# Optimization experiments

Measured on AMD Instinct MI355X. Metric: run time of the kernel, lower is better.

## Reference

```python
import jax, jax.numpy as jnp
import numpy as np

L = 3          # num_layer
EMB = 128      # emb_dim
NODE_F = 32    # node_feat_dim
EDGE_F = 16    # edge_feat_dim
TASKS = 1
N_GRAPHS = 64
EPS = 1e-5     # BatchNorm eps


def setup_inputs() -> dict:
    key = jax.random.key(0)
    ks = jax.random.split(key, 16)
    N, E = 50000, 800000
    x = jax.random.normal(ks[0], (N, NODE_F), dtype=jnp.float32)
    edge_index = jax.random.randint(ks[1], (2, E), 0, N, dtype=jnp.int32)
    edge_attr = jax.random.normal(ks[2], (E, EDGE_F), dtype=jnp.float32)
    batch = jnp.sort(jax.random.randint(ks[3], (N,), 0, N_GRAPHS, dtype=jnp.int32))
    s = lambda *sh: 1.0 / np.sqrt(sh[-1])
    # input node embedding
    W0 = jax.random.normal(ks[4], (EMB, NODE_F), dtype=jnp.float32) * s(EMB, NODE_F)
    b0 = jnp.zeros((EMB,), jnp.float32)
    # per-layer params, stacked over L
    We = jax.random.normal(ks[5], (L, EMB, EDGE_F), dtype=jnp.float32) * s(EMB, EDGE_F)
    be = jnp.zeros((L, EMB), jnp.float32)
    W1 = jax.random.normal(ks[6], (L, 2 * EMB, EMB), dtype=jnp.float32) * s(2 * EMB, EMB)
    b1 = jnp.zeros((L, 2 * EMB), jnp.float32)
    W2 = jax.random.normal(ks[7], (L, EMB, 2 * EMB), dtype=jnp.float32) * s(EMB, 2 * EMB)
    b2 = jnp.zeros((L, EMB), jnp.float32)
    gamma = jnp.ones((L, EMB), jnp.float32)
    beta = jnp.zeros((L, EMB), jnp.float32)
    # graph prediction head
    Wp = jax.random.normal(ks[8], (TASKS, EMB), dtype=jnp.float32) * s(TASKS, EMB)
    bp = jnp.zeros((TASKS,), jnp.float32)
    return {"x": x, "edge_attr": edge_attr, "W0": W0, "b0": b0, "We": We, "be": be,
            "W1": W1, "b1": b1, "W2": W2, "b2": b2, "gamma": gamma, "beta": beta,
            "Wp": Wp, "bp": bp, "edge_index": edge_index, "batch": batch}


def _forward(x, edge_attr, W0, b0, We, be, W1, b1, W2, b2, gamma, beta, Wp, bp,
             edge_index, batch):
    N = x.shape[0]
    src, dst = edge_index[0], edge_index[1]
    self_idx = jnp.arange(N, dtype=src.dtype)
    src_full = jnp.concatenate([src, self_idx])  # [E+N] with self loops
    dst_full = jnp.concatenate([dst, self_idx])
    h = x @ W0.T + b0  # [N, EMB]
    for l in range(L):
        # edge embedding; self-loop edge_attr is zeros -> embedding is just bias
        e_emb = edge_attr @ We[l].T + be[l]                       # [E, EMB]
        e_self = jnp.broadcast_to(be[l], (N, EMB))                # [N, EMB]
        msgs = h[src_full] + jnp.concatenate([e_emb, e_self], 0)  # [E+N, EMB]
        aggr = jax.ops.segment_sum(msgs, dst_full, num_segments=N)
        h2 = jax.nn.relu(aggr @ W1[l].T + b1[l]) @ W2[l].T + b2[l]
        # BatchNorm1d (training-mode batch statistics, biased var)
        mu = jnp.mean(h2, axis=0)
        var = jnp.mean(jnp.square(h2 - mu), axis=0)
        h = gamma[l] * (h2 - mu) * jax.lax.rsqrt(var + EPS) + beta[l]
        if l < L - 1:
            h = jax.nn.relu(h)
    # global mean pool over graphs
    sums = jax.ops.segment_sum(h, batch, num_segments=N_GRAPHS)
    cnts = jax.ops.segment_sum(jnp.ones((N,), h.dtype), batch, num_segments=N_GRAPHS)
    pooled = sums / jnp.maximum(cnts, 1.0)[:, None]
    return pooled @ Wp.T + bp  # [N_GRAPHS, TASKS]


def reference(x, edge_attr, W0, b0, We, be, W1, b1, W2, b2, gamma, beta, Wp, bp,
              edge_index, batch):
    return _forward(x, edge_attr, W0, b0, We, be, W1, b1, W2, b2, gamma, beta,
                    Wp, bp, edge_index, batch)
```

## Files before the change

### kernel.cpp

```cpp
#include <hip/hip_runtime.h>
#include <stdint.h>

#define EMB 128
#define LAYERS 3
#define NGRAPHS 64
#define BN_EPS 1e-5f

#define BSH 6
#define BNODES 64
#define SUBCAP 256
#define BCAP (8 * SUBCAP + 256)
#define OVFCAP 8192

typedef short short8 __attribute__((ext_vector_type(8)));
typedef float float4v __attribute__((ext_vector_type(4)));
typedef unsigned short ushort4v __attribute__((ext_vector_type(4)));

__device__ __forceinline__ unsigned short f2bf(float f) {
    union { float f; unsigned int i; } v; v.f = f;
    unsigned int x = v.i;
    unsigned int r = x + 0x7FFFu + ((x >> 16) & 1u);
    return (unsigned short)(r >> 16);
}
__device__ __forceinline__ float bflo(unsigned int u) {
    union { unsigned int i; float f; } v; v.i = u << 16; return v.f;
}
__device__ __forceinline__ float bfhi(unsigned int u) {
    union { unsigned int i; float f; } v; v.i = u & 0xffff0000u; return v.f;
}
__device__ __forceinline__ unsigned int packbf(float a, float b) {
    return (unsigned int)f2bf(a) | ((unsigned int)f2bf(b) << 16);
}

__global__ __launch_bounds__(256) void conv_bf16_3(
    const float* __restrict__ a, unsigned short* __restrict__ oa, int na,
    const float* __restrict__ b, unsigned short* __restrict__ ob, int nb,
    const float* __restrict__ c, unsigned short* __restrict__ oc, int nc)
{
    int i = blockIdx.x * 256 + threadIdx.x;
    int stride = gridDim.x * 256;
    for (int t = i; t < na + nb + nc; t += stride) {
        if (t < na) oa[t] = f2bf(a[t]);
        else if (t < na + nb) ob[t - na] = f2bf(b[t - na]);
        else oc[t - na - nb] = f2bf(c[t - na - nb]);
    }
}

template<int K, bool A_IS_BF16, bool RELU, bool OUT_BF16>
__global__ __launch_bounds__(256) void gemm_bt(
    const void* __restrict__ Av, const unsigned short* __restrict__ B,
    const float* __restrict__ bias, void* __restrict__ Cv,
    int M, int Ntot)
{
    const int wave = threadIdx.x >> 6;
    const int lane = threadIdx.x & 63;
    const int q    = lane >> 4;
    const int ln   = lane & 15;
    const int m_base = blockIdx.x * 64 + wave * 16;
    const int n_base = blockIdx.y * 64;

    float4v acc[4];
#pragma unroll
    for (int i = 0; i < 4; ++i) acc[i] = (float4v){0.f, 0.f, 0.f, 0.f};

    int mrow = m_base + ln;
    if (mrow >= M) mrow = M - 1;

    const int KSTEPS = K / 32;
#pragma unroll
    for (int ks = 0; ks < KSTEPS; ++ks) {
        const int k0 = ks * 32 + q * 8;
        short8 afrag;
        if constexpr (A_IS_BF16) {
            const unsigned short* A = (const unsigned short*)Av;
            afrag = *reinterpret_cast<const short8*>(A + (size_t)mrow * K + k0);
        } else {
            const float* A = (const float*)Av;
            const float4v* p = reinterpret_cast<const float4v*>(A + (size_t)mrow * K + k0);
            float4v f0 = p[0], f1 = p[1];
            afrag[0] = (short)f2bf(f0[0]); afrag[1] = (short)f2bf(f0[1]);
            afrag[2] = (short)f2bf(f0[2]); afrag[3] = (short)f2bf(f0[3]);
            afrag[4] = (short)f2bf(f1[0]); afrag[5] = (short)f2bf(f1[1]);
            afrag[6] = (short)f2bf(f1[2]); afrag[7] = (short)f2bf(f1[3]);
        }
#pragma unroll
        for (int nt = 0; nt < 4; ++nt) {
            const short8 bfrag = *reinterpret_cast<const short8*>(
                B + (size_t)(n_base + nt * 16 + ln) * K + k0);
            acc[nt] = __builtin_amdgcn_mfma_f32_16x16x32_bf16(afrag, bfrag, acc[nt], 0, 0, 0);
        }
    }

#pragma unroll
    for (int nt = 0; nt < 4; ++nt) {
        const int n = n_base + nt * 16 + ln;
        const float bv = bias[n];
#pragma unroll
        for (int r = 0; r < 4; ++r) {
            const int m = m_base + q * 4 + r;
            if (m < M) {
                float v = acc[nt][r] + bv;
                if constexpr (RELU) v = v > 0.f ? v : 0.f;
                if constexpr (OUT_BF16)
                    ((unsigned short*)Cv)[(size_t)m * Ntot + n] = f2bf(v);
                else
                    ((float*)Cv)[(size_t)m * Ntot + n] = v;
            }
        }
    }
}

__global__ __launch_bounds__(512) void fused_mlp(
    const unsigned short* __restrict__ ag, const unsigned short* __restrict__ W1,
    const float* __restrict__ b1, const unsigned short* __restrict__ W2,
    const float* __restrict__ b2, float* __restrict__ h2,
    float* __restrict__ sums2, int M, int ntiles)
{
    __shared__ unsigned short ag_lds[16 * 136];
    __shared__ unsigned short Ylds[16 * 264];
    const int tid = threadIdx.x;
    const int wave = tid >> 6, lane = tid & 63;
    const int q = lane >> 4, ln = lane & 15;
    const int k0 = q * 8;
    float* slice = sums2 + (size_t)(blockIdx.x & 31) * 256;

    short8 w1f[2][4], w2f[8];
#pragma unroll
    for (int c = 0; c < 2; ++c) {
        const int ct = wave * 2 + c;
#pragma unroll
        for (int ks = 0; ks < 4; ++ks)
            w1f[c][ks] = *reinterpret_cast<const short8*>(
                W1 + (size_t)(ct * 16 + ln) * 128 + ks * 32 + k0);
    }
#pragma unroll
    for (int ks = 0; ks < 8; ++ks)
        w2f[ks] = *reinterpret_cast<const short8*>(
            W2 + (size_t)(wave * 16 + ln) * 256 + ks * 32 + k0);
    float4v b1v[2];
    b1v[0] = *reinterpret_cast<const float4v*>(b1 + (wave * 2) * 16 + q * 4);
    b1v[1] = *reinterpret_cast<const float4v*>(b1 + (wave * 2 + 1) * 16 + q * 4);
    const float4v b2v = *reinterpret_cast<const float4v*>(b2 + wave * 16 + q * 4);

    for (int t = blockIdx.x; t < ntiles; t += gridDim.x) {
        const int nbase = t * 16;
        __syncthreads();
        {
            const int nd = tid >> 5, ch = (tid & 31) * 4;
            int ng = nbase + nd; if (ng >= M) ng = M - 1;
            *reinterpret_cast<uint2*>(&ag_lds[nd * 136 + ch]) =
                *reinterpret_cast<const uint2*>(ag + (size_t)ng * 128 + ch);
        }
        __syncthreads();

        short8 agf[4];
#pragma unroll
        for (int ks = 0; ks < 4; ++ks)
            agf[ks] = *reinterpret_cast<const short8*>(
                &ag_lds[ln * 136 + ks * 32 + k0]);
#pragma unroll
        for (int c = 0; c < 2; ++c) {
            float4v acc = (float4v){0.f, 0.f, 0.f, 0.f};
#pragma unroll
            for (int ks = 0; ks < 4; ++ks)
                acc = __builtin_amdgcn_mfma_f32_16x16x32_bf16(
                    w1f[c][ks], agf[ks], acc, 0, 0, 0);
            const int c0 = (wave * 2 + c) * 16 + q * 4;
            ushort4v pk;
            pk[0] = f2bf(fmaxf(acc[0] + b1v[c][0], 0.f));
            pk[1] = f2bf(fmaxf(acc[1] + b1v[c][1], 0.f));
            pk[2] = f2bf(fmaxf(acc[2] + b1v[c][2], 0.f));
            pk[3] = f2bf(fmaxf(acc[3] + b1v[c][3], 0.f));
            *reinterpret_cast<ushort4v*>(&Ylds[ln * 264 + c0]) = pk;
        }
        __syncthreads();

        short8 yf[8];
#pragma unroll
        for (int ks = 0; ks < 8; ++ks)
            yf[ks] = *reinterpret_cast<const short8*>(
                &Ylds[ln * 264 + ks * 32 + k0]);
        float4v acc = (float4v){0.f, 0.f, 0.f, 0.f};
#pragma unroll
        for (int ks = 0; ks < 8; ++ks)
            acc = __builtin_amdgcn_mfma_f32_16x16x32_bf16(
                w2f[ks], yf[ks], acc, 0, 0, 0);
        const int node = nbase + ln;
        const bool valid = (node < M);
        const int c0 = wave * 16 + q * 4;
        float4v v;
        v[0] = acc[0] + b2v[0]; v[1] = acc[1] + b2v[1];
        v[2] = acc[2] + b2v[2]; v[3] = acc[3] + b2v[3];
        if (valid)
            *reinterpret_cast<float4v*>(h2 + (size_t)node * 128 + c0) = v;

        float s[4], s2[4];
#pragma unroll
        for (int r = 0; r < 4; ++r) {
            const float x = valid ? v[r] : 0.f;
            s[r] = x; s2[r] = x * x;
        }
#pragma unroll
        for (int off = 1; off < 16; off <<= 1) {
#pragma unroll
            for (int r = 0; r < 4; ++r) {
                s[r]  += __shfl_xor(s[r],  off);
                s2[r] += __shfl_xor(s2[r], off);
            }
        }
        if (ln == 0) {
#pragma unroll
            for (int r = 0; r < 4; ++r) {
                atomicAdd(&slice[c0 + r], s[r]);
                atomicAdd(&slice[128 + c0 + r], s2[r]);
            }
        }
    }
}

__global__ __launch_bounds__(128) void bn_coef(
    const float* __restrict__ sums2, const float* __restrict__ gamma,
    const float* __restrict__ beta, float* __restrict__ coef, float invN)
{
    const int c = threadIdx.x;
    float s = 0.f, ss = 0.f;
    for (int k = 0; k < 32; ++k) {
        s  += sums2[k * 256 + c];
        ss += sums2[k * 256 + 128 + c];
    }
    float mu = s * invN;
    float var = ss * invN - mu * mu;
    float sc = gamma[c] * rsqrtf(fmaxf(var, 0.f) + BN_EPS);
    coef[c] = sc;
    coef[128 + c] = beta[c] - mu * sc;
}

__global__ __launch_bounds__(256) void edge_scatter(
    const int* __restrict__ ei, int* __restrict__ subcnt,
    uint2* __restrict__ staging, int* __restrict__ ovfcnt,
    uint4* __restrict__ ovfbuf, int E)
{
    const int sub = blockIdx.x & 7;
    const int e = blockIdx.x * 256 + threadIdx.x;
    if (e >= E) return;
    const unsigned int src = (unsigned int)ei[e];
    const int dst = ei[E + e];
    const int b = dst >> BSH;
    const unsigned int rx = src | ((unsigned int)(dst & (BNODES - 1)) << 16);
    const int sl = b * 8 + sub;
    const int pos = atomicAdd(&subcnt[sl], 1);
    if (pos < SUBCAP) {
        staging[(size_t)sl * SUBCAP + pos] = make_uint2(rx, (unsigned int)e);
    } else {
        int op = atomicAdd(ovfcnt, 1);
        if (op < OVFCAP)
            ovfbuf[op] = make_uint4(rx, (unsigned int)e, (unsigned int)b, 0u);
    }
}

__global__ __launch_bounds__(256) void bucket_scan(
    const int* __restrict__ subcnt, int* __restrict__ bucketbase, int B)
{
    const int t = threadIdx.x;
    int tot[4]; int mysum = 0;
#pragma unroll
    for (int j = 0; j < 4; ++j) {
        const int b = t * 4 + j;
        int s = 0;
        if (b < B)
            for (int k = 0; k < 8; ++k) s += subcnt[b * 8 + k];
        tot[j] = s; mysum += s;
    }
    const int lane = t & 63, wv = t >> 6;
    int iv = mysum;
#pragma unroll
    for (int off = 1; off < 64; off <<= 1) {
        int u = __shfl_up(iv, off);
        if (lane >= off) iv += u;
    }
    __shared__ int ws[4];
    if (lane == 63) ws[wv] = iv;
    __syncthreads();
    int woff = 0;
    for (int j = 0; j < wv; ++j) woff += ws[j];
    int ex = woff + iv - mysum;
#pragma unroll
    for (int j = 0; j < 4; ++j) {
        const int b = t * 4 + j;
        if (b < B) bucketbase[b] = ex;
        ex += tot[j];
    }
    if (t == 255) bucketbase[B] = ex;
}

__global__ __launch_bounds__(256) void csr_build(
    const int* __restrict__ subcnt, const int* __restrict__ bucketbase,
    const uint2* __restrict__ staging, const int* __restrict__ ovfcnt,
    const uint4* __restrict__ ovfbuf,
    int2* __restrict__ adj, int* __restrict__ rowptr, int N, int E)
{
    __shared__ uint2 recs[BCAP];
    __shared__ int scnt[8], sp[8], cnt[BNODES], rp_s[BNODES], wp2[BNODES];
    __shared__ int totsh;
    const int b = blockIdx.x;
    const int tid = threadIdx.x;
    if (tid < 8) scnt[tid] = min(subcnt[b * 8 + tid], SUBCAP);
    if (tid < BNODES) cnt[tid] = 0;
    __syncthreads();
    if (tid == 0) {
        int a = 0;
        for (int s = 0; s < 8; ++s) { sp[s] = a; a += scnt[s]; }
        totsh = a;
    }
    __syncthreads();
    for (int s = 0; s < 8; ++s) {
        const int L = scnt[s];
        const uint2* srcp = staging + (size_t)(b * 8 + s) * SUBCAP;
        for (int i = tid; i < L; i += 256) {
            uint2 r = srcp[i];
            recs[sp[s] + i] = r;
            atomicAdd(&cnt[(r.x >> 16) & (BNODES - 1)], 1);
        }
    }
    __syncthreads();
    const int ov = min(*ovfcnt, OVFCAP);
    if (ov > 0) {
        for (int i = tid; i < ov; i += 256) {
            uint4 r = ovfbuf[i];
            if ((int)r.z == b) {
                int p = atomicAdd(&totsh, 1);
                if (p < BCAP) {
                    recs[p] = make_uint2(r.x, r.y);
                    atomicAdd(&cnt[(r.x >> 16) & (BNODES - 1)], 1);
                }
            }
        }
    }
    __syncthreads();
    const int total = min(totsh, BCAP);
    if (tid < BNODES) {
        int v = cnt[tid];
        int iv = v;
#pragma unroll
        for (int off = 1; off < 64; off <<= 1) {
            int u = __shfl_up(iv, off);
            if (tid >= off) iv += u;
        }
        rp_s[tid] = iv - v;
        wp2[tid] = 0;
    }
    __syncthreads();
    const int base = bucketbase[b];
    const int n0 = b * BNODES;
    const int nn = min(BNODES, N - n0);
    if (tid < nn) rowptr[n0 + tid] = base + rp_s[tid];
    if (b == 0 && tid == 0) rowptr[N] = E;
    for (int i = tid; i < total; i += 256) {
        uint2 r = recs[i];
        const int d = (r.x >> 16) & (BNODES - 1);
        const int pos = rp_s[d] + atomicAdd(&wp2[d], 1);
        adj[base + pos] = make_int2((int)(r.x & 0xFFFFu), (int)r.y);
    }
}

__global__ __launch_bounds__(256) void mom_gather(
    const int2* __restrict__ adj, const int* __restrict__ rowptr,
    const float* __restrict__ eattr, float* __restrict__ mom, int N)
{
    const int lane = threadIdx.x & 63;
    const int gwave = (blockIdx.x * 256 + threadIdx.x) >> 6;
    const int nwaves = (gridDim.x * 256) >> 6;
    const int j = lane >> 4, k = lane & 15;
    for (int n = gwave; n < N; n += nwaves) {
        const int s = rowptr[n], e = rowptr[n + 1];
        float acc = 0.f;
        for (int p = s + j; p < e; p += 4) {
            const int eid = adj[p].y;
            acc += eattr[(size_t)eid * 16 + k];
        }
        acc += __shfl_xor(acc, 16);
        acc += __shfl_xor(acc, 32);
        if (lane < 16) mom[(size_t)n * 16 + lane] = acc;
    }
}

__global__ __launch_bounds__(256) void aggregate_kernel(
    const unsigned short* __restrict__ h, const int2* __restrict__ adj,
    const int* __restrict__ rowptr, const float* __restrict__ mom,
    const float* __restrict__ We, const float* __restrict__ be,
    unsigned short* __restrict__ ag, int N)
{
    const int lane = threadIdx.x & 63;
    const int gwave = (blockIdx.x * 256 + threadIdx.x) >> 6;
    const int nwaves = (gridDim.x * 256) >> 6;
    const int c0 = 2 * lane;

    float w0[16], w1[16];
#pragma unroll
    for (int k = 0; k < 16; ++k) {
        w0[k] = We[c0 * 16 + k];
        w1[k] = We[(c0 + 1) * 16 + k];
    }
    const float b0 = be[c0], b1 = be[c0 + 1];

    for (int n = gwave; n < N; n += nwaves) {
        const int s = rowptr[n], e = rowptr[n + 1];
        unsigned int self = *reinterpret_cast<const unsigned int*>(
            h + (size_t)n * 128 + c0);
        float ax = bflo(self), ay = bfhi(self);
        float mval = (lane < 16) ? mom[(size_t)n * 16 + lane] : 0.f;

        int p = s;
        for (; p + 16 <= e; p += 16) {
            int idx[16];
#pragma unroll
            for (int j = 0; j < 16; ++j) idx[j] = adj[p + j].x;
            unsigned int vv[16];
#pragma unroll
            for (int j = 0; j < 16; ++j)
                vv[j] = *reinterpret_cast<const unsigned int*>(
                    h + (size_t)idx[j] * 128 + c0);
#pragma unroll
            for (int j = 0; j < 16; ++j) { ax += bflo(vv[j]); ay += bfhi(vv[j]); }
        }
        if (p < e) {
            const int last = e - 1;
            int idx[16];
#pragma unroll
            for (int j = 0; j < 16; ++j) {
                int pp = p + j;
                idx[j] = adj[pp < e ? pp : last].x;
            }
            unsigned int vv[16];
#pragma unroll
            for (int j = 0; j < 16; ++j)
                vv[j] = *reinterpret_cast<const unsigned int*>(
                    h + (size_t)idx[j] * 128 + c0);
#pragma unroll
            for (int j = 0; j < 16; ++j) {
                if (p + j < e) { ax += bflo(vv[j]); ay += bfhi(vv[j]); }
            }
        }

        const float degp1 = (float)(e - s + 1);
        float d0 = b0 * degp1, d1 = b1 * degp1;
#pragma unroll
        for (int k = 0; k < 16; ++k) {
            const float sk = __shfl(mval, k);
            d0 += w0[k] * sk; d1 += w1[k] * sk;
        }
        ax += d0; ay += d1;
        *reinterpret_cast<unsigned int*>(ag + (size_t)n * 128 + c0) = packbf(ax, ay);
    }
}

__global__ __launch_bounds__(256) void bn_apply_bf16(
    const float* __restrict__ h2, const float* __restrict__ coef,
    unsigned short* __restrict__ h, int total4)
{
    int tid = blockIdx.x * 256 + threadIdx.x;
    int c4 = (tid * 4) & 127;
    float sc[4], sh[4];
#pragma unroll
    for (int j = 0; j < 4; ++j) {
        sc[j] = coef[c4 + j];
        sh[j] = coef[128 + c4 + j];
    }
    int stride = gridDim.x * 256;
    for (int i = tid; i < total4; i += stride) {
        float4v v = reinterpret_cast<const float4v*>(h2)[i];
        float x0 = fmaxf(sc[0] * v[0] + sh[0], 0.f);
        float x1 = fmaxf(sc[1] * v[1] + sh[1], 0.f);
        float x2 = fmaxf(sc[2] * v[2] + sh[2], 0.f);
        float x3 = fmaxf(sc[3] * v[3] + sh[3], 0.f);
        uint2 o; o.x = packbf(x0, x1); o.y = packbf(x2, x3);
        reinterpret_cast<uint2*>(h)[i] = o;
    }
}

__global__ __launch_bounds__(256) void pool_part(
    const float* __restrict__ h2, const int* __restrict__ batch,
    float* __restrict__ pooled, int N)
{
    const int per = (N + gridDim.x - 1) / gridDim.x;
    const int start = blockIdx.x * per;
    const int end = min(start + per, N);
    if (start >= end) return;
    const int c = threadIdx.x & 127;
    const int sub = threadIdx.x >> 7;
    int g_cur = batch[start];
    float acc = 0.f;
    for (int n = start + sub; n < end; n += 2) {
        int g = batch[n];
        if (g != g_cur) {
            if (acc != 0.f) atomicAdd(&pooled[(size_t)g_cur * 128 + c], acc);
            acc = 0.f; g_cur = g;
        }
        acc += h2[(size_t)n * 128 + c];
    }
    if (acc != 0.f) atomicAdd(&pooled[(size_t)g_cur * 128 + c], acc);
}

__global__ __launch_bounds__(128) void head_final(
    const float* __restrict__ pooled, const int* __restrict__ batch,
    const float* __restrict__ coef, const float* __restrict__ Wp,
    const float* __restrict__ bp, float* __restrict__ out, int N)
{
    const int g = blockIdx.x;
    __shared__ int sb[2];
    if (threadIdx.x < 2) {
        int target = g + threadIdx.x;
        int lo = 0, hi = N;
        while (lo < hi) {
            int mid = (lo + hi) >> 1;
            if (batch[mid] < target) lo = mid + 1; else hi = mid;
        }
        sb[threadIdx.x] = lo;
    }
    __syncthreads();
    const float cntf = fmaxf((float)(sb[1] - sb[0]), 1.f);
    const int c = threadIdx.x;
    float m = pooled[(size_t)g * 128 + c] / cntf;
    float v = (coef[c] * m + coef[128 + c]) * Wp[c];
    const int lane = threadIdx.x & 63;
#pragma unroll
    for (int off = 32; off > 0; off >>= 1) v += __shfl_down(v, off);
    __shared__ float wsum[2];
    if (lane == 0) wsum[threadIdx.x >> 6] = v;
    __syncthreads();
    if (threadIdx.x == 0) out[g] = wsum[0] + wsum[1] + bp[0];
}

extern "C" void kernel_launch(void* const* d_in, const int* in_sizes, int n_in,
                              void* d_out, int out_size, void* d_ws, size_t ws_size,
                              hipStream_t stream)
{
    const float* x     = (const float*)d_in[0];
    const float* eattr = (const float*)d_in[1];
    const float* W0    = (const float*)d_in[2];
    const float* b0    = (const float*)d_in[3];
    const float* We    = (const float*)d_in[4];
    const float* be    = (const float*)d_in[5];
    const float* W1    = (const float*)d_in[6];
    const float* b1    = (const float*)d_in[7];
    const float* W2    = (const float*)d_in[8];
    const float* b2    = (const float*)d_in[9];
    const float* gamma = (const float*)d_in[10];
    const float* beta  = (const float*)d_in[11];
    const float* Wp    = (const float*)d_in[12];
    const float* bp    = (const float*)d_in[13];
    const int* ei    = (const int*)d_in[14];
    const int* batch = (const int*)d_in[15];

    const int N = in_sizes[0] / 32;
    const int E = in_sizes[1] / 16;
    const int NB = (N + BNODES - 1) / BNODES;

    char* ws = (char*)d_ws;
    size_t off = 0;
    auto alloc = [&](size_t bytes) { char* p = ws + off; off += (bytes + 255) & ~(size_t)255; return p; };
    unsigned short* hb = (unsigned short*)alloc((size_t)N * 128 * 2);
    unsigned short* ag = (unsigned short*)alloc((size_t)N * 128 * 2);
    float* h2 = (float*)alloc((size_t)N * 128 * 4);
    uint2* staging = (uint2*)h2;
    float* sums2   = (float*)alloc(32 * 256 * 4);
    float* coef    = (float*)alloc(256 * 4);
    float* pooled  = (float*)alloc(NGRAPHS * 128 * 4);
    float* mom     = (float*)alloc((size_t)N * 16 * 4);
    unsigned short* W0bf = (unsigned short*)alloc(128 * 32 * 2);
    unsigned short* W1bf = (unsigned short*)alloc(3 * 256 * 128 * 2);
    unsigned short* W2bf = (unsigned short*)alloc(3 * 128 * 256 * 2);
    int* rowptr   = (int*)alloc(((size_t)N + 1) * 4);
    int* subcnt   = (int*)alloc(((size_t)NB * 8 + 1) * 4);
    int* ovfcnt   = subcnt + NB * 8;
    int* bucketbase = (int*)alloc(((size_t)NB + 1) * 4);
    uint4* ovfbuf = (uint4*)alloc((size_t)OVFCAP * 16);
    int2* adj     = (int2*)alloc((size_t)E * 8);

    const dim3 blk(256);
    const int mblocks = (N + 63) / 64;
    const int ntiles = (N + 15) / 16;
    const int total4 = N * 32;
    const int eblocks = (E + 255) / 256;
    const float invN = 1.0f / (float)N;

    hipMemsetAsync(subcnt, 0, ((size_t)NB * 8 + 1) * 4, stream);
    edge_scatter<<<dim3(eblocks), blk, 0, stream>>>(
        ei, subcnt, staging, ovfcnt, ovfbuf, E);
    bucket_scan<<<dim3(1), blk, 0, stream>>>(subcnt, bucketbase, NB);
    csr_build<<<dim3(NB), blk, 0, stream>>>(
        subcnt, bucketbase, staging, ovfcnt, ovfbuf, adj, rowptr, N, E);
    mom_gather<<<dim3(2048), blk, 0, stream>>>(adj, rowptr, eattr, mom, N);

    conv_bf16_3<<<dim3(384), blk, 0, stream>>>(
        W0, W0bf, 128 * 32, W1, W1bf, 3 * 256 * 128, W2, W2bf, 3 * 128 * 256);

    gemm_bt<32, false, false, true><<<dim3(mblocks, 2), blk, 0, stream>>>(
        x, W0bf, b0, (void*)hb, N, 128);

    for (int l = 0; l < LAYERS; ++l) {
        hipMemsetAsync(sums2, 0, 32 * 256 * 4, stream);
        aggregate_kernel<<<dim3(2048), blk, 0, stream>>>(
            hb, adj, rowptr, mom, We + l * 128 * 16, be + l * 128, ag, N);
        fused_mlp<<<dim3(640), dim3(512), 0, stream>>>(
            ag, W1bf + l * 256 * 128, b1 + l * 256,
            W2bf + l * 128 * 256, b2 + l * 128, h2, sums2, N, ntiles);
        bn_coef<<<dim3(1), dim3(128), 0, stream>>>(
            sums2, gamma + l * 128, beta + l * 128, coef, invN);
        if (l < LAYERS - 1)
            bn_apply_bf16<<<dim3(1024), blk, 0, stream>>>(h2, coef, hb, total4);
    }

    hipMemsetAsync(pooled, 0, NGRAPHS * 128 * 4, stream);
    pool_part<<<dim3(784), blk, 0, stream>>>(h2, batch, pooled, N);
    head_final<<<dim3(NGRAPHS), dim3(128), 0, stream>>>(
        pooled, batch, coef, Wp, bp, (float*)d_out, N);
}
```

Baseline: 508.6 us.

## Process 32-node tiles in fused MLP and pad gather tail with zero row

The fused MLP kernel now handles two 16-node subtiles per iteration. That halves the barriers and the per-tile atomic BN-statistic reductions per node, widens the LDS staging loads, and sizes the grid so each block does about three tiles. The aggregate kernel's tail loop now runs in chunks of 8, and out-of-range indices point to an extra zeroed row N of h, which is cleared once by a memset. This removes per-element predication and the redundant loads of the last element. It costs more LDS per block and fewer blocks in flight.

```diff
diff --git a/kernel.cpp b/kernel.cpp
--- a/kernel.cpp
+++ b/kernel.cpp
@@ -116,8 +116,8 @@
     const float* __restrict__ b2, float* __restrict__ h2,
     float* __restrict__ sums2, int M, int ntiles)
 {
-    __shared__ unsigned short ag_lds[16 * 136];
-    __shared__ unsigned short Ylds[16 * 264];
+    __shared__ unsigned short ag_lds[32 * 136];
+    __shared__ unsigned short Ylds[32 * 264];
     const int tid = threadIdx.x;
     const int wave = tid >> 6, lane = tid & 63;
     const int q = lane >> 4, ln = lane & 15;
@@ -143,62 +143,69 @@
     const float4v b2v = *reinterpret_cast<const float4v*>(b2 + wave * 16 + q * 4);
 
     for (int t = blockIdx.x; t < ntiles; t += gridDim.x) {
-        const int nbase = t * 16;
+        const int nbase = t * 32;
         __syncthreads();
         {
-            const int nd = tid >> 5, ch = (tid & 31) * 4;
+            const int nd = tid >> 4, ch = (tid & 15) * 8;
             int ng = nbase + nd; if (ng >= M) ng = M - 1;
-            *reinterpret_cast<uint2*>(&ag_lds[nd * 136 + ch]) =
-                *reinterpret_cast<const uint2*>(ag + (size_t)ng * 128 + ch);
+            *reinterpret_cast<uint4*>(&ag_lds[nd * 136 + ch]) =
+                *reinterpret_cast<const uint4*>(ag + (size_t)ng * 128 + ch);
         }
         __syncthreads();
 
-        short8 agf[4];
-#pragma unroll
-        for (int ks = 0; ks < 4; ++ks)
-            agf[ks] = *reinterpret_cast<const short8*>(
-                &ag_lds[ln * 136 + ks * 32 + k0]);
-#pragma unroll
-        for (int c = 0; c < 2; ++c) {
+#pragma unroll
+        for (int nt = 0; nt < 2; ++nt) {
+            short8 agf[4];
+#pragma unroll
+            for (int ks = 0; ks < 4; ++ks)
+                agf[ks] = *reinterpret_cast<const short8*>(
+                    &ag_lds[(nt * 16 + ln) * 136 + ks * 32 + k0]);
+#pragma unroll
+            for (int c = 0; c < 2; ++c) {
+                float4v acc = (float4v){0.f, 0.f, 0.f, 0.f};
+#pragma unroll
+                for (int ks = 0; ks < 4; ++ks)
+                    acc = __builtin_amdgcn_mfma_f32_16x16x32_bf16(
+                        w1f[c][ks], agf[ks], acc, 0, 0, 0);
+                const int c0 = (wave * 2 + c) * 16 + q * 4;
+                ushort4v pk;
+                pk[0] = f2bf(fmaxf(acc[0] + b1v[c][0], 0.f));
+                pk[1] = f2bf(fmaxf(acc[1] + b1v[c][1], 0.f));
+                pk[2] = f2bf(fmaxf(acc[2] + b1v[c][2], 0.f));
+                pk[3] = f2bf(fmaxf(acc[3] + b1v[c][3], 0.f));
+                *reinterpret_cast<ushort4v*>(&Ylds[(nt * 16 + ln) * 264 + c0]) = pk;
+            }
+        }
+        __syncthreads();
+
+        float s[4], s2[4];
+#pragma unroll
+        for (int r = 0; r < 4; ++r) { s[r] = 0.f; s2[r] = 0.f; }
+        const int c0 = wave * 16 + q * 4;
+#pragma unroll
+        for (int nt = 0; nt < 2; ++nt) {
+            short8 yf[8];
+#pragma unroll
+            for (int ks = 0; ks < 8; ++ks)
+                yf[ks] = *reinterpret_cast<const short8*>(
+                    &Ylds[(nt * 16 + ln) * 264 + ks * 32 + k0]);
             float4v acc = (float4v){0.f, 0.f, 0.f, 0.f};
 #pragma unroll
-            for (int ks = 0; ks < 4; ++ks)
+            for (int ks = 0; ks < 8; ++ks)
                 acc = __builtin_amdgcn_mfma_f32_16x16x32_bf16(
-                    w1f[c][ks], agf[ks], acc, 0, 0, 0);
-            const int c0 = (wave * 2 + c) * 16 + q * 4;
-            ushort4v pk;
-            pk[0] = f2bf(fmaxf(acc[0] + b1v[c][0], 0.f));
-            pk[1] = f2bf(fmaxf(acc[1] + b1v[c][1], 0.f));
-            pk[2] = f2bf(fmaxf(acc[2] + b1v[c][2], 0.f));
-            pk[3] = f2bf(fmaxf(acc[3] + b1v[c][3], 0.f));
-            *reinterpret_cast<ushort4v*>(&Ylds[ln * 264 + c0]) = pk;
-        }
-        __syncthreads();
-
-        short8 yf[8];
-#pragma unroll
-        for (int ks = 0; ks < 8; ++ks)
-            yf[ks] = *reinterpret_cast<const short8*>(
-                &Ylds[ln * 264 + ks * 32 + k0]);
-        float4v acc = (float4v){0.f, 0.f, 0.f, 0.f};
-#pragma unroll
-        for (int ks = 0; ks < 8; ++ks)
-            acc = __builtin_amdgcn_mfma_f32_16x16x32_bf16(
-                w2f[ks], yf[ks], acc, 0, 0, 0);
-        const int node = nbase + ln;
-        const bool valid = (node < M);
-        const int c0 = wave * 16 + q * 4;
-        float4v v;
-        v[0] = acc[0] + b2v[0]; v[1] = acc[1] + b2v[1];
-        v[2] = acc[2] + b2v[2]; v[3] = acc[3] + b2v[3];
-        if (valid)
-            *reinterpret_cast<float4v*>(h2 + (size_t)node * 128 + c0) = v;
-
-        float s[4], s2[4];
-#pragma unroll
-        for (int r = 0; r < 4; ++r) {
-            const float x = valid ? v[r] : 0.f;
-            s[r] = x; s2[r] = x * x;
+                    w2f[ks], yf[ks], acc, 0, 0, 0);
+            const int node = nbase + nt * 16 + ln;
+            const bool valid = (node < M);
+            float4v v;
+            v[0] = acc[0] + b2v[0]; v[1] = acc[1] + b2v[1];
+            v[2] = acc[2] + b2v[2]; v[3] = acc[3] + b2v[3];
+            if (valid)
+                *reinterpret_cast<float4v*>(h2 + (size_t)node * 128 + c0) = v;
+#pragma unroll
+            for (int r = 0; r < 4; ++r) {
+                const float x = valid ? v[r] : 0.f;
+                s[r] += x; s2[r] += x * x;
+            }
         }
 #pragma unroll
         for (int off = 1; off < 16; off <<= 1) {
@@ -423,23 +430,20 @@
 #pragma unroll
             for (int j = 0; j < 16; ++j) { ax += bflo(vv[j]); ay += bfhi(vv[j]); }
         }
-        if (p < e) {
-            const int last = e - 1;
-            int idx[16];
-#pragma unroll
-            for (int j = 0; j < 16; ++j) {
-                int pp = p + j;
-                idx[j] = adj[pp < e ? pp : last].x;
+        for (; p < e; p += 8) {
+            int idx[8];
+#pragma unroll
+            for (int j = 0; j < 8; ++j) {
+                const int pp = p + j;
+                idx[j] = (pp < e) ? adj[pp].x : N;
             }
-            unsigned int vv[16];
-#pragma unroll
-            for (int j = 0; j < 16; ++j)
+            unsigned int vv[8];
+#pragma unroll
+            for (int j = 0; j < 8; ++j)
                 vv[j] = *reinterpret_cast<const unsigned int*>(
                     h + (size_t)idx[j] * 128 + c0);
 #pragma unroll
-            for (int j = 0; j < 16; ++j) {
-                if (p + j < e) { ax += bflo(vv[j]); ay += bfhi(vv[j]); }
-            }
+            for (int j = 0; j < 8; ++j) { ax += bflo(vv[j]); ay += bfhi(vv[j]); }
         }
 
         const float degp1 = (float)(e - s + 1);
@@ -559,7 +563,7 @@
     char* ws = (char*)d_ws;
     size_t off = 0;
     auto alloc = [&](size_t bytes) { char* p = ws + off; off += (bytes + 255) & ~(size_t)255; return p; };
-    unsigned short* hb = (unsigned short*)alloc((size_t)N * 128 * 2);
+    unsigned short* hb = (unsigned short*)alloc((size_t)(N + 1) * 128 * 2);
     unsigned short* ag = (unsigned short*)alloc((size_t)N * 128 * 2);
     float* h2 = (float*)alloc((size_t)N * 128 * 4);
     uint2* staging = (uint2*)h2;
@@ -579,12 +583,14 @@
 
     const dim3 blk(256);
     const int mblocks = (N + 63) / 64;
-    const int ntiles = (N + 15) / 16;
+    const int mtiles = (N + 31) / 32;
+    const int fblocks = (mtiles + 2) / 3;
     const int total4 = N * 32;
     const int eblocks = (E + 255) / 256;
     const float invN = 1.0f / (float)N;
 
     hipMemsetAsync(subcnt, 0, ((size_t)NB * 8 + 1) * 4, stream);
+    hipMemsetAsync(hb + (size_t)N * 128, 0, 128 * 2, stream);
     edge_scatter<<<dim3(eblocks), blk, 0, stream>>>(
         ei, subcnt, staging, ovfcnt, ovfbuf, E);
     bucket_scan<<<dim3(1), blk, 0, stream>>>(subcnt, bucketbase, NB);
@@ -602,9 +608,9 @@
         hipMemsetAsync(sums2, 0, 32 * 256 * 4, stream);
         aggregate_kernel<<<dim3(2048), blk, 0, stream>>>(
             hb, adj, rowptr, mom, We + l * 128 * 16, be + l * 128, ag, N);
-        fused_mlp<<<dim3(640), dim3(512), 0, stream>>>(
+        fused_mlp<<<dim3(fblocks), dim3(512), 0, stream>>>(
             ag, W1bf + l * 256 * 128, b1 + l * 256,
-            W2bf + l * 128 * 256, b2 + l * 128, h2, sums2, N, ntiles);
+            W2bf + l * 128 * 256, b2 + l * 128, h2, sums2, N, mtiles);
         bn_coef<<<dim3(1), dim3(128), 0, stream>>>(
             sums2, gamma + l * 128, beta + l * 128, coef, invN);
         if (l < LAYERS - 1)
```

Result: faster. 471.2 us (-7.4%).
